# Performance work log

Measured on AMD Instinct MI355X. Metric: run time of the kernel, lower is better.

Reference implementation:

```python
import jax, jax.numpy as jnp
import numpy as np

N_NODES = 50000
N_EDGES = 800000
D = 128


def setup_inputs() -> dict:
    key = jax.random.key(0)
    ks = jax.random.split(key, 5)
    x = jax.random.normal(ks[0], (N_NODES, D), dtype=jnp.float32)
    edge_index = jax.random.randint(ks[1], (2, N_EDGES), 0, N_NODES, dtype=jnp.int64)
    # GCNConv linear weight + bias, and the two DGCN parameters
    Wc = jax.random.normal(ks[2], (D, D), dtype=jnp.float32) / np.sqrt(D)
    bc = jnp.zeros((D,), dtype=jnp.float32)
    W0 = jax.random.normal(ks[3], (D, D), dtype=jnp.float32)
    Wt = jax.random.normal(ks[4], (D, D), dtype=jnp.float32)
    return {"x": x, "edge_index": edge_index, "Wc": Wc, "bc": bc, "W0": W0, "Wt": Wt}


def gcn_conv(x, edge_index, Wc, bc):
    # PyG GCNConv: add self-loops, symmetric normalization D^-1/2 (A+I) D^-1/2,
    # applied to x @ Wc, plus bias.
    n = x.shape[0]
    loops = jnp.arange(n, dtype=edge_index.dtype)
    src = jnp.concatenate([edge_index[0], loops])  # [E+N]
    dst = jnp.concatenate([edge_index[1], loops])
    ones = jnp.ones(src.shape[0], dtype=x.dtype)
    deg = jax.ops.segment_sum(ones, dst, num_segments=n)  # in-degree incl. self-loop
    dinv = jnp.where(deg > 0, jax.lax.rsqrt(deg), 0.0)
    norm = dinv[src] * dinv[dst]  # [E+N]
    xw = x @ Wc  # [N, D]
    msgs = xw[src] * norm[:, None]  # gather + scale  [E+N, D]
    agg = jax.ops.segment_sum(msgs, dst, num_segments=n)  # scatter-add  [N, D]
    return agg + bc


def reference(x, edge_index, Wc, bc, W0, Wt):
    h_neigh = gcn_conv(x, edge_index, Wc, bc)
    h_self = x @ W0
    h_change = (h_neigh - x) @ Wt
    return h_neigh + h_self + h_change
```

## Files before the change

kernel.cpp:

```cpp
#include <hip/hip_runtime.h>

#define N_NODES 50000
#define N_EDGES 800000
#define D 128
#define NB 391
#define CAPB 4928
#define P1B 256
#define EPB ((N_EDGES + P1B - 1) / P1B)
#define CAP 28
#define WPB 16
#define XC0 (P1B + WPB + 1)
#define KA_BLOCKS (XC0 + (N_NODES * 16) / 256)

typedef __attribute__((ext_vector_type(8))) short short8;
typedef __attribute__((ext_vector_type(4))) float f32x4;

__device__ __forceinline__ unsigned short f2bf(float f) {
    unsigned int u = __builtin_bit_cast(unsigned int, f);
    u += 0x7FFFu + ((u >> 16) & 1u);
    return (unsigned short)(u >> 16);
}
__device__ __forceinline__ float bf2f(unsigned short h) {
    unsigned int u = ((unsigned int)h) << 16;
    return __builtin_bit_cast(float, u);
}

__global__ void k_init(int* __restrict__ gcur) {
    const int t = threadIdx.x;
    if (t < NB) gcur[t] = 0;
}

__global__ __launch_bounds__(256) void k_a(const int* __restrict__ src,
                                           const int* __restrict__ dst,
                                           int* __restrict__ gcur,
                                           unsigned int* __restrict__ pbuf,
                                           const float* __restrict__ Wc,
                                           const float* __restrict__ W0,
                                           const float* __restrict__ Wt,
                                           const float* __restrict__ bc,
                                           const float* __restrict__ x,
                                           unsigned short* __restrict__ Wp,
                                           float* __restrict__ bv,
                                           unsigned short* __restrict__ xb) {
    __shared__ float sWt[D * D];
    const int t = threadIdx.x;
    const unsigned int bid = blockIdx.x;

    if (bid < P1B) {
        unsigned int (*stage)[CAP + 1] =
            reinterpret_cast<unsigned int(*)[CAP + 1]>(sWt);
        int* scnt = reinterpret_cast<int*>(sWt) + NB * (CAP + 1);
        for (int i = t; i < NB; i += 256) scnt[i] = 0;
        __syncthreads();

        const long e0 = (long)bid * EPB;
        const long e1 = (e0 + EPB < N_EDGES) ? e0 + EPB : N_EDGES;
        for (long e = e0 + t; e < e1; e += 256) {
            const int s = src[e];
            const int d = dst[e];
            const int b = d >> 7;
            const unsigned int p = ((unsigned int)(d & 127) << 16) | (unsigned int)s;
            const int slot = atomicAdd(&scnt[b], 1);
            if (slot < CAP) {
                stage[b][slot] = p;
            } else {
                pbuf[(long)b * CAPB + atomicAdd(&gcur[b], 1)] = p;
            }
        }
        __syncthreads();
        for (int bb = t; bb < NB; bb += 256) {
            const int n = (scnt[bb] < CAP) ? scnt[bb] : CAP;
            if (n > 0) {
                const int pos = bb * CAPB + atomicAdd(&gcur[bb], n);
                for (int i = 0; i < n; ++i) pbuf[pos + i] = stage[bb][i];
            }
        }
        return;
    }

    if (bid < P1B + WPB) {
        for (int i = t * 4; i < D * D; i += 256 * 4)
            *(float4*)(sWt + i) = *(const float4*)(Wt + i);
        __syncthreads();
        const int id = (int)(bid - P1B) * 256 + t;
        const int lane = id & 63;
        const int tile = (id >> 6) & 7;
        const int step = id >> 9;
        const int n = tile * 16 + (lane & 15);
        const int kbase = step * 32 + (lane >> 4) * 8;
        unsigned short v[8];
#pragma unroll
        for (int j = 0; j < 8; ++j) {
            const int k = kbase + j;
            float f;
            if (k < D) {
                f = Wc[k * D + n];
#pragma unroll 16
                for (int m = 0; m < D; ++m) f += Wc[k * D + m] * sWt[m * D + n];
            } else {
                f = W0[(k - D) * D + n] - sWt[(k - D) * D + n];
            }
            v[j] = f2bf(f);
        }
        *(uint4*)(Wp + (long)id * 8) = *(uint4*)v;
        return;
    }

    if (bid == P1B + WPB) {
        if (t < D) {
            float acc = bc[t];
#pragma unroll 16
            for (int k = 0; k < D; ++k) acc += bc[k] * Wt[k * D + t];
            bv[t] = acc;
        }
        return;
    }

    const int gid = (int)(bid - XC0) * 256 + t;
    const int node = gid >> 4;
    const int c = gid & 15;
    const float4 a = ((const float4*)x)[(long)node * 32 + c * 2];
    const float4 b = ((const float4*)x)[(long)node * 32 + c * 2 + 1];
    const float f[8] = {a.x, a.y, a.z, a.w, b.x, b.y, b.z, b.w};
    unsigned short vb[8];
#pragma unroll
    for (int j = 0; j < 8; ++j) vb[j] = f2bf(f[j]);
    *(uint4*)(xb + (long)node * 128 + c * 8) = *(uint4*)vb;
}

__global__ __launch_bounds__(256) void k_part2(const unsigned int* __restrict__ pbuf,
                                               const int* __restrict__ gcur,
                                               int* __restrict__ row_start,
                                               int* __restrict__ cnt,
                                               float* __restrict__ dinv,
                                               int* __restrict__ esrc) {
    __shared__ int lcnt[128];
    __shared__ int lcur[128];
    __shared__ int stmp[128];
    const int b = blockIdx.x;
    const int t = threadIdx.x;
    const int base = b * CAPB;
    const int n = gcur[b];

    if (t < 128) lcnt[t] = 0;
    __syncthreads();
    for (int i = t; i < n; i += 256) atomicAdd(&lcnt[pbuf[base + i] >> 16], 1);
    __syncthreads();

    int c = 0;
    if (t < 128) {
        c = lcnt[t];
        stmp[t] = c;
    }
    __syncthreads();
    for (int off = 1; off < 128; off <<= 1) {
        int u = (t >= off && t < 128) ? stmp[t - off] : 0;
        __syncthreads();
        if (t < 128) stmp[t] += u;
        __syncthreads();
    }
    if (t < 128) {
        const int ls = base + stmp[t] - c;
        lcur[t] = ls;
        const int node = b * 128 + t;
        if (node < N_NODES) {
            row_start[node] = ls;
            cnt[node] = c;
            dinv[node] = rsqrtf((float)c + 1.0f);
        }
    }
    __syncthreads();

    for (int i = t; i < n; i += 256) {
        const unsigned int p = pbuf[base + i];
        const int pos = atomicAdd(&lcur[p >> 16], 1);
        esrc[pos] = (int)(p & 0xFFFFu);
    }
}

__global__ __launch_bounds__(256) void k_gmm(const unsigned short* __restrict__ xb,
                                             const int* __restrict__ row_start,
                                             const int* __restrict__ cnt,
                                             const float* __restrict__ dinv,
                                             const int* __restrict__ esrc,
                                             const unsigned short* __restrict__ Wp,
                                             const float* __restrict__ bv,
                                             float* __restrict__ out) {
    __shared__ unsigned short sg[64 * 128];
    const int tid = threadIdx.x;
    const int wave = tid >> 6;
    const int lane = tid & 63;
    const int c = lane & 15;
    const int s = lane >> 4;
    const int row0 = blockIdx.x * 64;

    for (int m = 0; m < 16; ++m) {
        const int node = row0 + wave * 16 + m;
        const bool valid = node < N_NODES;
        float acc[8] = {};
        if (valid) {
            const int begin = row_start[node];
            const int end = begin + cnt[node];
            int i = begin + s;
            for (; i + 12 < end; i += 16) {
                const int a0 = esrc[i];
                const int a1 = esrc[i + 4];
                const int a2 = esrc[i + 8];
                const int a3 = esrc[i + 12];
                const short8 v0 = *(const short8*)(xb + (long)a0 * 128 + c * 8);
                const short8 v1 = *(const short8*)(xb + (long)a1 * 128 + c * 8);
                const short8 v2 = *(const short8*)(xb + (long)a2 * 128 + c * 8);
                const short8 v3 = *(const short8*)(xb + (long)a3 * 128 + c * 8);
                const float d0 = dinv[a0];
                const float d1 = dinv[a1];
                const float d2 = dinv[a2];
                const float d3 = dinv[a3];
#pragma unroll
                for (int j = 0; j < 8; ++j)
                    acc[j] += (d0 * bf2f((unsigned short)v0[j]) +
                               d1 * bf2f((unsigned short)v1[j])) +
                              (d2 * bf2f((unsigned short)v2[j]) +
                               d3 * bf2f((unsigned short)v3[j]));
            }
            for (; i < end; i += 4) {
                const int a0 = esrc[i];
                const float d0 = dinv[a0];
                const short8 v0 = *(const short8*)(xb + (long)a0 * 128 + c * 8);
#pragma unroll
                for (int j = 0; j < 8; ++j) acc[j] += d0 * bf2f((unsigned short)v0[j]);
            }
        }
#pragma unroll
        for (int j = 0; j < 8; ++j) {
            acc[j] += __shfl_xor(acc[j], 16);
            acc[j] += __shfl_xor(acc[j], 32);
        }
        if (s == 0) {
            const int r = wave * 16 + m;
            unsigned short o[8] = {0, 0, 0, 0, 0, 0, 0, 0};
            if (valid) {
                const float di = dinv[node];
                const short8 xs = *(const short8*)(xb + (long)node * 128 + c * 8);
#pragma unroll
                for (int j = 0; j < 8; ++j)
                    o[j] = f2bf(di * (acc[j] + di * bf2f((unsigned short)xs[j])));
            }
            const int col = (c * 16) ^ ((r & 7) << 4);
            *(uint4*)((char*)sg + r * 256 + col) = *(uint4*)o;
        }
    }
    __syncthreads();

    const int lr = lane & 15;
    const int quad = lane >> 4;
    const int rloc = wave * 16 + lr;
    int ar = row0 + rloc;
    if (ar >= N_NODES) ar = N_NODES - 1;
    const unsigned short* aptr = xb + (long)ar * 128 + quad * 8;

    f32x4 acc2[8] = {};
#pragma unroll
    for (int s8 = 0; s8 < 8; ++s8) {
        short8 a;
        if (s8 < 4) {
            const int colb = (s8 * 64 + quad * 16) ^ ((rloc & 7) << 4);
            a = *(const short8*)((const char*)sg + rloc * 256 + colb);
        } else {
            a = *(const short8*)(aptr + (s8 - 4) * 32);
        }
#pragma unroll
        for (int t2 = 0; t2 < 8; ++t2) {
            const short8 b =
                *(const short8*)(Wp + ((long)(s8 * 8 + t2) * 64 + lane) * 8);
            acc2[t2] = __builtin_amdgcn_mfma_f32_16x16x32_bf16(a, b, acc2[t2], 0, 0, 0);
        }
    }

    const int rowbase = row0 + wave * 16;
#pragma unroll
    for (int t2 = 0; t2 < 8; ++t2) {
        const int col = t2 * 16 + lr;
        const float bvv = bv[col];
#pragma unroll
        for (int r = 0; r < 4; ++r) {
            const int row = rowbase + quad * 4 + r;
            if (row < N_NODES) out[(long)row * D + col] = acc2[t2][r] + bvv;
        }
    }
}

extern "C" void kernel_launch(void* const* d_in, const int* in_sizes, int n_in,
                              void* d_out, int out_size, void* d_ws, size_t ws_size,
                              hipStream_t stream) {
    const float* x  = (const float*)d_in[0];
    const int*   ei = (const int*)d_in[1];
    const float* Wc = (const float*)d_in[2];
    const float* bc = (const float*)d_in[3];
    const float* W0 = (const float*)d_in[4];
    const float* Wt = (const float*)d_in[5];
    float* out = (float*)d_out;

    const int* src = ei;
    const int* dst = ei + N_EDGES;

    unsigned short* xb = (unsigned short*)d_ws;
    int*   cnt        = (int*)(xb + (size_t)N_NODES * 128);
    int*   row_start  = cnt + N_NODES;
    float* dinv       = (float*)(row_start + N_NODES);
    int*   esrc       = (int*)(dinv + N_NODES);
    unsigned int* pbuf = (unsigned int*)(esrc + (size_t)NB * CAPB);
    float* bv         = (float*)(pbuf + (size_t)NB * CAPB);
    unsigned short* Wp = (unsigned short*)(bv + D);
    int*   gcur       = (int*)(Wp + 256 * D);

    k_init<<<1, 512, 0, stream>>>(gcur);
    k_a<<<KA_BLOCKS, 256, 0, stream>>>(src, dst, gcur, pbuf, Wc, W0, Wt, bc, x,
                                       Wp, bv, xb);
    k_part2<<<NB, 256, 0, stream>>>(pbuf, gcur, row_start, cnt, dinv, esrc);
    k_gmm<<<(N_NODES + 63) / 64, 256, 0, stream>>>(xb, row_start, cnt, dinv, esrc,
                                                   Wp, bv, out);
}
```

Baseline: 182.3 us.

## Double k_gmm block to 512 threads, split MFMA columns across waves, shrink k_a LDS

k_gmm now runs 8 waves per 64-row block. Each wave gathers 8 nodes instead of 16, with the row ranges preloaded, and the MFMA stage is split so each wave computes 4 of the 8 column tiles. This aims to raise parallelism and latency hiding for the gather-bound aggregation. In k_a, the 64KB shared Wt buffer is removed: the weight-fold blocks read Wt from global and reuse it across 8 outputs, and the staging CAP drops to 16. The smaller LDS footprint lets more k_a blocks fit per CU, at the cost of more global-atomic spills from the smaller staging buffer.

```diff
diff --git a/kernel.cpp b/kernel.cpp
--- a/kernel.cpp
+++ b/kernel.cpp
@@ -7,7 +7,7 @@
 #define CAPB 4928
 #define P1B 256
 #define EPB ((N_EDGES + P1B - 1) / P1B)
-#define CAP 28
+#define CAP 16
 #define WPB 16
 #define XC0 (P1B + WPB + 1)
 #define KA_BLOCKS (XC0 + (N_NODES * 16) / 256)
@@ -42,14 +42,12 @@
                                            unsigned short* __restrict__ Wp,
                                            float* __restrict__ bv,
                                            unsigned short* __restrict__ xb) {
-    __shared__ float sWt[D * D];
+    __shared__ unsigned int stage[NB][CAP + 1];
+    __shared__ int scnt[NB];
     const int t = threadIdx.x;
     const unsigned int bid = blockIdx.x;
 
     if (bid < P1B) {
-        unsigned int (*stage)[CAP + 1] =
-            reinterpret_cast<unsigned int(*)[CAP + 1]>(sWt);
-        int* scnt = reinterpret_cast<int*>(sWt) + NB * (CAP + 1);
         for (int i = t; i < NB; i += 256) scnt[i] = 0;
         __syncthreads();
 
@@ -79,29 +77,30 @@
     }
 
     if (bid < P1B + WPB) {
-        for (int i = t * 4; i < D * D; i += 256 * 4)
-            *(float4*)(sWt + i) = *(const float4*)(Wt + i);
-        __syncthreads();
         const int id = (int)(bid - P1B) * 256 + t;
         const int lane = id & 63;
         const int tile = (id >> 6) & 7;
         const int step = id >> 9;
         const int n = tile * 16 + (lane & 15);
         const int kbase = step * 32 + (lane >> 4) * 8;
-        unsigned short v[8];
+        float f[8];
 #pragma unroll
         for (int j = 0; j < 8; ++j) {
             const int k = kbase + j;
-            float f;
-            if (k < D) {
-                f = Wc[k * D + n];
-#pragma unroll 16
-                for (int m = 0; m < D; ++m) f += Wc[k * D + m] * sWt[m * D + n];
-            } else {
-                f = W0[(k - D) * D + n] - sWt[(k - D) * D + n];
+            f[j] = (k < D) ? Wc[k * D + n]
+                           : (W0[(k - D) * D + n] - Wt[(k - D) * D + n]);
+        }
+        if (kbase < D) {
+#pragma unroll 8
+            for (int m = 0; m < D; ++m) {
+                const float wt = Wt[m * D + n];
+#pragma unroll
+                for (int j = 0; j < 8; ++j) f[j] += Wc[(kbase + j) * D + m] * wt;
             }
-            v[j] = f2bf(f);
-        }
+        }
+        unsigned short v[8];
+#pragma unroll
+        for (int j = 0; j < 8; ++j) v[j] = f2bf(f[j]);
         *(uint4*)(Wp + (long)id * 8) = *(uint4*)v;
         return;
     }
@@ -178,7 +177,7 @@
     }
 }
 
-__global__ __launch_bounds__(256) void k_gmm(const unsigned short* __restrict__ xb,
+__global__ __launch_bounds__(512) void k_gmm(const unsigned short* __restrict__ xb,
                                              const int* __restrict__ row_start,
                                              const int* __restrict__ cnt,
                                              const float* __restrict__ dinv,
@@ -194,41 +193,49 @@
     const int s = lane >> 4;
     const int row0 = blockIdx.x * 64;
 
-    for (int m = 0; m < 16; ++m) {
-        const int node = row0 + wave * 16 + m;
+    int beg[8], en[8];
+#pragma unroll
+    for (int m = 0; m < 8; ++m) {
+        const int node = row0 + wave * 8 + m;
+        const bool v = node < N_NODES;
+        const int b0 = v ? row_start[node] : 0;
+        beg[m] = b0;
+        en[m] = b0 + (v ? cnt[node] : 0);
+    }
+
+#pragma unroll
+    for (int m = 0; m < 8; ++m) {
+        const int node = row0 + wave * 8 + m;
         const bool valid = node < N_NODES;
         float acc[8] = {};
-        if (valid) {
-            const int begin = row_start[node];
-            const int end = begin + cnt[node];
-            int i = begin + s;
-            for (; i + 12 < end; i += 16) {
-                const int a0 = esrc[i];
-                const int a1 = esrc[i + 4];
-                const int a2 = esrc[i + 8];
-                const int a3 = esrc[i + 12];
-                const short8 v0 = *(const short8*)(xb + (long)a0 * 128 + c * 8);
-                const short8 v1 = *(const short8*)(xb + (long)a1 * 128 + c * 8);
-                const short8 v2 = *(const short8*)(xb + (long)a2 * 128 + c * 8);
-                const short8 v3 = *(const short8*)(xb + (long)a3 * 128 + c * 8);
-                const float d0 = dinv[a0];
-                const float d1 = dinv[a1];
-                const float d2 = dinv[a2];
-                const float d3 = dinv[a3];
-#pragma unroll
-                for (int j = 0; j < 8; ++j)
-                    acc[j] += (d0 * bf2f((unsigned short)v0[j]) +
-                               d1 * bf2f((unsigned short)v1[j])) +
-                              (d2 * bf2f((unsigned short)v2[j]) +
-                               d3 * bf2f((unsigned short)v3[j]));
-            }
-            for (; i < end; i += 4) {
-                const int a0 = esrc[i];
-                const float d0 = dinv[a0];
-                const short8 v0 = *(const short8*)(xb + (long)a0 * 128 + c * 8);
-#pragma unroll
-                for (int j = 0; j < 8; ++j) acc[j] += d0 * bf2f((unsigned short)v0[j]);
-            }
+        int i = beg[m] + s;
+        const int end = en[m];
+        for (; i + 12 < end; i += 16) {
+            const int a0 = esrc[i];
+            const int a1 = esrc[i + 4];
+            const int a2 = esrc[i + 8];
+            const int a3 = esrc[i + 12];
+            const short8 v0 = *(const short8*)(xb + (long)a0 * 128 + c * 8);
+            const short8 v1 = *(const short8*)(xb + (long)a1 * 128 + c * 8);
+            const short8 v2 = *(const short8*)(xb + (long)a2 * 128 + c * 8);
+            const short8 v3 = *(const short8*)(xb + (long)a3 * 128 + c * 8);
+            const float d0 = dinv[a0];
+            const float d1 = dinv[a1];
+            const float d2 = dinv[a2];
+            const float d3 = dinv[a3];
+#pragma unroll
+            for (int j = 0; j < 8; ++j)
+                acc[j] += (d0 * bf2f((unsigned short)v0[j]) +
+                           d1 * bf2f((unsigned short)v1[j])) +
+                          (d2 * bf2f((unsigned short)v2[j]) +
+                           d3 * bf2f((unsigned short)v3[j]));
+        }
+        for (; i < end; i += 4) {
+            const int a0 = esrc[i];
+            const float d0 = dinv[a0];
+            const short8 v0 = *(const short8*)(xb + (long)a0 * 128 + c * 8);
+#pragma unroll
+            for (int j = 0; j < 8; ++j) acc[j] += d0 * bf2f((unsigned short)v0[j]);
         }
 #pragma unroll
         for (int j = 0; j < 8; ++j) {
@@ -236,7 +243,7 @@
             acc[j] += __shfl_xor(acc[j], 32);
         }
         if (s == 0) {
-            const int r = wave * 16 + m;
+            const int r = wave * 8 + m;
             unsigned short o[8] = {0, 0, 0, 0, 0, 0, 0, 0};
             if (valid) {
                 const float di = dinv[node];
@@ -253,12 +260,14 @@
 
     const int lr = lane & 15;
     const int quad = lane >> 4;
-    const int rloc = wave * 16 + lr;
+    const int wr = wave & 3;
+    const int wc = wave >> 2;
+    const int rloc = wr * 16 + lr;
     int ar = row0 + rloc;
     if (ar >= N_NODES) ar = N_NODES - 1;
     const unsigned short* aptr = xb + (long)ar * 128 + quad * 8;
 
-    f32x4 acc2[8] = {};
+    f32x4 acc2[4] = {};
 #pragma unroll
     for (int s8 = 0; s8 < 8; ++s8) {
         short8 a;
@@ -269,17 +278,17 @@
             a = *(const short8*)(aptr + (s8 - 4) * 32);
         }
 #pragma unroll
-        for (int t2 = 0; t2 < 8; ++t2) {
+        for (int t2 = 0; t2 < 4; ++t2) {
             const short8 b =
-                *(const short8*)(Wp + ((long)(s8 * 8 + t2) * 64 + lane) * 8);
+                *(const short8*)(Wp + ((long)(s8 * 8 + wc * 4 + t2) * 64 + lane) * 8);
             acc2[t2] = __builtin_amdgcn_mfma_f32_16x16x32_bf16(a, b, acc2[t2], 0, 0, 0);
         }
     }
 
-    const int rowbase = row0 + wave * 16;
-#pragma unroll
-    for (int t2 = 0; t2 < 8; ++t2) {
-        const int col = t2 * 16 + lr;
+    const int rowbase = row0 + wr * 16;
+#pragma unroll
+    for (int t2 = 0; t2 < 4; ++t2) {
+        const int col = wc * 64 + t2 * 16 + lr;
         const float bvv = bv[col];
 #pragma unroll
         for (int r = 0; r < 4; ++r) {
@@ -317,6 +326,6 @@
     k_a<<<KA_BLOCKS, 256, 0, stream>>>(src, dst, gcur, pbuf, Wc, W0, Wt, bc, x,
                                        Wp, bv, xb);
     k_part2<<<NB, 256, 0, stream>>>(pbuf, gcur, row_start, cnt, dinv, esrc);
-    k_gmm<<<(N_NODES + 63) / 64, 256, 0, stream>>>(xb, row_start, cnt, dinv, esrc,
+    k_gmm<<<(N_NODES + 63) / 64, 512, 0, stream>>>(xb, row_start, cnt, dinv, esrc,
                                                    Wp, bv, out);
 }
```

New measurement: 176.2 us. 3.3% less time.
